# Performance work log

Hardware: AMD Instinct MI355X
Metric: run time of the kernel (lower is better)

The kernel has to match this reference:

```python
import jax, jax.numpy as jnp
import numpy as np

K, B, D, H = 8, 8192, 1024, 256


def setup_inputs() -> dict:
    key = jax.random.key(0)
    k_x, k_w1, k_w2 = jax.random.split(key, 3)
    x = jax.random.normal(k_x, (B, D), dtype=jnp.float32)
    # He-ish scaled weights so reconstructions stay finite
    W1 = jax.random.normal(k_w1, (K, D, H), dtype=jnp.float32) * (1.0 / np.sqrt(D))
    b1 = jnp.zeros((K, H), dtype=jnp.float32)
    W2 = jax.random.normal(k_w2, (K, H, D), dtype=jnp.float32) * (1.0 / np.sqrt(H))
    b2 = jnp.zeros((K, D), dtype=jnp.float32)
    return {"x": x, "W1": W1, "b1": b1, "W2": W2, "b2": b2}


def reference(x, W1, b1, W2, b2):
    # Run every expert AE on the full batch (matches predict()):
    h = jax.nn.relu(jnp.einsum('bd,kdh->kbh', x, W1) + b1[:, None, :])   # [K,B,H]
    recon = jnp.einsum('kbh,khd->kbd', h, W2) + b2[:, None, :]            # [K,B,D]
    # per-sample reconstruction MSE per expert
    err = jnp.mean((recon - x[None]) ** 2, axis=-1)                       # [K,B]
    # cluster_assignment = argmax over (-err) == argmin over err
    assign = jnp.argmin(err, axis=0)                                      # [B] int
    # gather-compute-scatter: select the winning expert's reconstruction
    x_out = recon[assign, jnp.arange(recon.shape[1])]                     # [B,D]
    return x_out
```

## Files before the change

kernel.cpp:

```cpp
#include <hip/hip_runtime.h>


#define KE 8
#define NB 8192
#define ND 1024
#define NH 256

typedef float f32x4 __attribute__((ext_vector_type(4)));
typedef short s16x8 __attribute__((ext_vector_type(8)));
typedef unsigned short u16x8 __attribute__((ext_vector_type(8)));
typedef unsigned short u16x4 __attribute__((ext_vector_type(4)));

__device__ __forceinline__ float bf2f(unsigned short h) {
  union { unsigned int u; float f; } v; v.u = ((unsigned int)h) << 16; return v.f;
}
__device__ __forceinline__ unsigned short f2bf(float f) {
  union { unsigned int u; float f; } v; v.f = f;
  unsigned int u = v.u;
  u += 0x7fffu + ((u >> 16) & 1u);
  return (unsigned short)(u >> 16);
}
__device__ __forceinline__ void split2(float x, unsigned short& hi, unsigned short& lo) {
  hi = f2bf(x);
  lo = f2bf(x - bf2f(hi));
}

__global__ __launch_bounds__(256) void pack_all(
    const float* __restrict__ W1, unsigned short* __restrict__ w1oh, unsigned short* __restrict__ w1ol,
    const float* __restrict__ W2, unsigned short* __restrict__ w2oh, unsigned short* __restrict__ w2ol,
    const float* __restrict__ xin, unsigned short* __restrict__ xoh, unsigned short* __restrict__ xol,
    unsigned int* __restrict__ cnt) {
  const int bx = blockIdx.x;
  const int tid = threadIdx.x;
  if (bx == 0 && tid < KE) cnt[tid] = 0;

  if (bx < 1024) {
    int gid = bx * 256 + tid;
    int L = gid & 63;
    int g = gid >> 6;
    int ks = g & 31;
    int ct = (g >> 5) & 15;
    int k = g >> 9;
    int col = ct * 16 + (L & 15);
    int kd0 = ks * 32 + (L >> 4) * 8;
    unsigned short th[8], tl[8];
#pragma unroll
    for (int j = 0; j < 8; ++j) {
      float v = W1[((size_t)k * ND + kd0 + j) * NH + col];
      split2(v, th[j], tl[j]);
    }
    size_t o = ((size_t)g * 64 + L) * 8;
    *(u16x8*)&w1oh[o] = *(u16x8*)th;
    *(u16x8*)&w1ol[o] = *(u16x8*)tl;
  } else if (bx < 2048) {
    int gid = (bx - 1024) * 256 + tid;
    int L = gid & 63;
    int g = gid >> 6;
    int ks = g & 7;
    int dt = (g >> 3) & 63;
    int k = g >> 9;
    int d2 = dt * 16 + (L & 15);
    int h0 = ks * 32 + (L >> 4) * 8;
    unsigned short th[8], tl[8];
#pragma unroll
    for (int j = 0; j < 8; ++j) {
      float v = W2[((size_t)k * NH + h0 + j) * ND + d2];
      split2(v, th[j], tl[j]);
    }
    size_t o = ((size_t)g * 64 + L) * 8;
    *(u16x8*)&w2oh[o] = *(u16x8*)th;
    *(u16x8*)&w2ol[o] = *(u16x8*)tl;
  } else {
    int gid = (bx - 2048) * 256 + tid;
    int L = gid & 63;
    int g = gid >> 6;
    int ks = g & 31;
    int rt = g >> 5;
    int row = rt * 16 + (L & 15);
    int kd0 = ks * 32 + (L >> 4) * 8;
    float4 a = *(const float4*)&xin[(size_t)row * ND + kd0];
    float4 b = *(const float4*)&xin[(size_t)row * ND + kd0 + 4];
    unsigned short th[8], tl[8];
    split2(a.x, th[0], tl[0]); split2(a.y, th[1], tl[1]);
    split2(a.z, th[2], tl[2]); split2(a.w, th[3], tl[3]);
    split2(b.x, th[4], tl[4]); split2(b.y, th[5], tl[5]);
    split2(b.z, th[6], tl[6]); split2(b.w, th[7], tl[7]);
    size_t o = ((size_t)g * 64 + L) * 8;
    *(u16x8*)&xoh[o] = *(u16x8*)th;
    *(u16x8*)&xol[o] = *(u16x8*)tl;
  }
}

#define LOAD_STAGE(ah, al, bh, bl, it)                  \
  do {                                                  \
    _Pragma("unroll")                                   \
    for (int q_ = 0; q_ < 4; ++q_) {                    \
      int o_ = xo[q_] + (it) * 512;                     \
      ah[q_] = *(const s16x8*)&xph[o_];                 \
      al[q_] = *(const s16x8*)&xpl[o_];                 \
    }                                                   \
    _Pragma("unroll")                                   \
    for (int q_ = 0; q_ < 4; ++q_) {                    \
      int o_ = wo1[q_] + (it) * 512;                    \
      bh[q_] = *(const s16x8*)&w1ph[o_];                \
      bl[q_] = *(const s16x8*)&w1pl[o_];                \
    }                                                   \
  } while (0)

#define MFMA_STAGE(ah, al, bh, bl)                                                                   \
  do {                                                                                               \
    _Pragma("unroll")                                                                                \
    for (int nt_ = 0; nt_ < 4; ++nt_)                                                                \
      _Pragma("unroll")                                                                              \
      for (int mt_ = 0; mt_ < 4; ++mt_) {                                                            \
        acc1[mt_][nt_] = __builtin_amdgcn_mfma_f32_16x16x32_bf16(ah[mt_], bh[nt_], acc1[mt_][nt_], 0, 0, 0); \
        acc1[mt_][nt_] = __builtin_amdgcn_mfma_f32_16x16x32_bf16(ah[mt_], bl[nt_], acc1[mt_][nt_], 0, 0, 0); \
        acc1[mt_][nt_] = __builtin_amdgcn_mfma_f32_16x16x32_bf16(al[mt_], bh[nt_], acc1[mt_][nt_], 0, 0, 0); \
      }                                                                                              \
  } while (0)

__global__ __launch_bounds__(256, 2) void ae_pass1(
    const unsigned short* __restrict__ xph, const unsigned short* __restrict__ xpl,
    const float* __restrict__ x,
    const unsigned short* __restrict__ w1ph, const unsigned short* __restrict__ w1pl,
    const float* __restrict__ b1,
    const unsigned short* __restrict__ w2ph, const unsigned short* __restrict__ w2pl,
    const float* __restrict__ b2, float* __restrict__ err) {
  __shared__ union {
    struct { unsigned short h[64][256]; unsigned short l[64][256]; } hs;
    float errp[4][64];
  } s;

  const int tid = threadIdx.x;
  const int wv = tid >> 6;
  const int lane = tid & 63;
  const int lo = lane & 15;
  const int quad = lane >> 4;
  const int k = blockIdx.x & 7;
  const int rtile = blockIdx.x >> 3;
  const int r0 = rtile * 64;

  int xo[4], wo1[4];
#pragma unroll
  for (int mt = 0; mt < 4; ++mt) xo[mt] = ((rtile * 4 + mt) * 32) * 512 + lane * 8;
#pragma unroll
  for (int nt = 0; nt < 4; ++nt) wo1[nt] = ((k * 16 + wv * 4 + nt) * 32) * 512 + lane * 8;

  f32x4 acc1[4][4];
#pragma unroll
  for (int mt = 0; mt < 4; ++mt)
#pragma unroll
    for (int nt = 0; nt < 4; ++nt) acc1[mt][nt] = (f32x4){0.f, 0.f, 0.f, 0.f};

  s16x8 Aah[4], Aal[4], Abh[4], Abl[4];
  s16x8 Bah[4], Bal[4], Bbh[4], Bbl[4];
  LOAD_STAGE(Aah, Aal, Abh, Abl, 0);
  LOAD_STAGE(Bah, Bal, Bbh, Bbl, 1);
  for (int it = 0; it < 32; it += 2) {
    MFMA_STAGE(Aah, Aal, Abh, Abl);
    if (it + 2 < 32) LOAD_STAGE(Aah, Aal, Abh, Abl, it + 2);
    MFMA_STAGE(Bah, Bal, Bbh, Bbl);
    if (it + 3 < 32) LOAD_STAGE(Bah, Bal, Bbh, Bbl, it + 3);
  }

#pragma unroll
  for (int nt = 0; nt < 4; ++nt) {
    float b1v = b1[(size_t)k * NH + wv * 64 + nt * 16 + lo];
#pragma unroll
    for (int mt = 0; mt < 4; ++mt)
#pragma unroll
      for (int i = 0; i < 4; ++i) {
        float v = acc1[mt][nt][i] + b1v;
        v = v > 0.f ? v : 0.f;
        unsigned short vh, vl;
        split2(v, vh, vl);
        int row = mt * 16 + quad * 4 + i, col = wv * 64 + nt * 16 + lo;
        int sc = col ^ ((row & 7) << 3);
        s.hs.h[row][sc] = vh;
        s.hs.l[row][sc] = vl;
      }
  }
  __syncthreads();

  float eacc[4][4];
#pragma unroll
  for (int mt = 0; mt < 4; ++mt)
#pragma unroll
    for (int i = 0; i < 4; ++i) eacc[mt][i] = 0.f;

  const int w2base = ((k * 64 + wv * 16) * 8) * 512 + lane * 8;

  for (int mc = 0; mc < 2; ++mc) {
    s16x8 hh[2][8], hl[2][8];
#pragma unroll
    for (int m2 = 0; m2 < 2; ++m2) {
      int row = (mc * 2 + m2) * 16 + lo;
      int rbase = row * 256;
      int sw = (row & 7) << 3;
#pragma unroll
      for (int ks = 0; ks < 8; ++ks) {
        int off = rbase + ((ks * 32 + quad * 8) ^ sw);
        hh[m2][ks] = *(const s16x8*)(&s.hs.h[0][0] + off);
        hl[m2][ks] = *(const s16x8*)(&s.hs.l[0][0] + off);
      }
    }
    for (int dt = 0; dt < 16; ++dt) {
      f32x4 acc2[2];
      acc2[0] = (f32x4){0.f, 0.f, 0.f, 0.f};
      acc2[1] = (f32x4){0.f, 0.f, 0.f, 0.f};
#pragma unroll
      for (int ks = 0; ks < 8; ++ks) {
        int wo = w2base + dt * 4096 + ks * 512;
        s16x8 bh = *(const s16x8*)&w2ph[wo];
        s16x8 bl = *(const s16x8*)&w2pl[wo];
#pragma unroll
        for (int m2 = 0; m2 < 2; ++m2) {
          acc2[m2] = __builtin_amdgcn_mfma_f32_16x16x32_bf16(hh[m2][ks], bh, acc2[m2], 0, 0, 0);
          acc2[m2] = __builtin_amdgcn_mfma_f32_16x16x32_bf16(hh[m2][ks], bl, acc2[m2], 0, 0, 0);
          acc2[m2] = __builtin_amdgcn_mfma_f32_16x16x32_bf16(hl[m2][ks], bh, acc2[m2], 0, 0, 0);
        }
      }
      const int d2 = wv * 256 + dt * 16 + lo;
      float b2v = b2[(size_t)k * ND + d2];
#pragma unroll
      for (int m2 = 0; m2 < 2; ++m2)
#pragma unroll
        for (int i = 0; i < 4; ++i) {
          int row = (mc * 2 + m2) * 16 + quad * 4 + i;
          float rec = acc2[m2][i] + b2v;
          float xv = x[(size_t)(r0 + row) * ND + d2];
          float dd = rec - xv;
          eacc[mc * 2 + m2][i] += dd * dd;
        }
    }
  }

  __syncthreads();
#pragma unroll
  for (int mt = 0; mt < 4; ++mt)
#pragma unroll
    for (int i = 0; i < 4; ++i) {
      float v = eacc[mt][i];
      v += __shfl_xor(v, 1, 16);
      v += __shfl_xor(v, 2, 16);
      v += __shfl_xor(v, 4, 16);
      v += __shfl_xor(v, 8, 16);
      if (lo == 0) s.errp[wv][mt * 16 + quad * 4 + i] = v;
    }
  __syncthreads();
  if (tid < 64)
    err[(size_t)k * NB + r0 + tid] =
        (s.errp[0][tid] + s.errp[1][tid] + s.errp[2][tid] + s.errp[3][tid]) * (1.0f / (float)ND);
}

__global__ __launch_bounds__(256) void ae_argmin(const float* __restrict__ err,
                                                 unsigned int* __restrict__ cnt,
                                                 int* __restrict__ bucket) {
  __shared__ unsigned int lc[KE];
  __shared__ unsigned int base[KE];
  int tid = threadIdx.x;
  if (tid < KE) lc[tid] = 0;
  __syncthreads();
  int b = blockIdx.x * 256 + tid;
  float best = err[b];
  int kmin = 0;
#pragma unroll
  for (int j = 1; j < KE; ++j) {
    float e = err[(size_t)j * NB + b];
    if (e < best) { best = e; kmin = j; }
  }
  unsigned int lpos = atomicAdd(&lc[kmin], 1u);
  __syncthreads();
  if (tid < KE) base[tid] = atomicAdd(&cnt[tid], lc[tid]);
  __syncthreads();
  bucket[(size_t)kmin * NB + (int)(base[kmin] + lpos)] = b;
}

__global__ __launch_bounds__(256) void ae_pass2(
    const float* __restrict__ x,
    const unsigned short* __restrict__ w1ph, const float* __restrict__ b1,
    const unsigned short* __restrict__ w2ph, const float* __restrict__ b2,
    const unsigned int* __restrict__ cnt, const int* __restrict__ bucket,
    float* __restrict__ out) {
  __shared__ unsigned short hs[64][NH + 8];
  __shared__ unsigned short xs[64][40];
  __shared__ int rid[64];

  const int k = blockIdx.x & 7;
  const int cv = (int)cnt[k];
  const int t0 = (blockIdx.x >> 3) * 64;
  if (t0 >= cv) return;
  const int nrows = min(64, cv - t0);

  const int tid = threadIdx.x;
  const int wv = tid >> 6;
  const int lane = tid & 63;
  const int lo = lane & 15;
  const int quad = lane >> 4;
  const int srow = tid >> 2, scol = (tid & 3) * 8;

  if (tid < 64) {
    int idx = t0 + tid;
    rid[tid] = bucket[(size_t)k * NB + (idx < cv ? idx : t0)];
  }
  __syncthreads();
  const int grow = rid[srow];

  f32x4 acc1[4][4];
#pragma unroll
  for (int mt = 0; mt < 4; ++mt)
#pragma unroll
    for (int nt = 0; nt < 4; ++nt) acc1[mt][nt] = (f32x4){0.f, 0.f, 0.f, 0.f};

  for (int it = 0; it < 32; ++it) {
    float4 xa = *(const float4*)&x[(size_t)grow * ND + it * 32 + scol];
    float4 xb = *(const float4*)&x[(size_t)grow * ND + it * 32 + scol + 4];
    s16x8 bfr[4];
#pragma unroll
    for (int nt = 0; nt < 4; ++nt)
      bfr[nt] = *(const s16x8*)&w1ph[(((size_t)(k * 16 + wv * 4 + nt) * 32) + it) * 512 + lane * 8];
    __syncthreads();
    unsigned short t[8];
    t[0] = f2bf(xa.x); t[1] = f2bf(xa.y); t[2] = f2bf(xa.z); t[3] = f2bf(xa.w);
    t[4] = f2bf(xb.x); t[5] = f2bf(xb.y); t[6] = f2bf(xb.z); t[7] = f2bf(xb.w);
    *(u16x8*)&xs[srow][scol] = *(u16x8*)t;
    __syncthreads();
    s16x8 af[4];
#pragma unroll
    for (int mt = 0; mt < 4; ++mt) af[mt] = *(const s16x8*)&xs[mt * 16 + lo][quad * 8];
#pragma unroll
    for (int mt = 0; mt < 4; ++mt)
#pragma unroll
      for (int nt = 0; nt < 4; ++nt)
        acc1[mt][nt] = __builtin_amdgcn_mfma_f32_16x16x32_bf16(af[mt], bfr[nt], acc1[mt][nt], 0, 0, 0);
  }
  __syncthreads();

#pragma unroll
  for (int nt = 0; nt < 4; ++nt) {
    float b1v = b1[(size_t)k * NH + wv * 64 + nt * 16 + lo];
#pragma unroll
    for (int mt = 0; mt < 4; ++mt)
#pragma unroll
      for (int i = 0; i < 4; ++i) {
        float v = acc1[mt][nt][i] + b1v;
        v = v > 0.f ? v : 0.f;
        hs[mt * 16 + quad * 4 + i][wv * 64 + nt * 16 + lo] = f2bf(v);
      }
  }
  __syncthreads();

  for (int c = 0; c < 32; ++c) {
    f32x4 acc2[2];
    acc2[0] = (f32x4){0.f, 0.f, 0.f, 0.f};
    acc2[1] = (f32x4){0.f, 0.f, 0.f, 0.f};
#pragma unroll
    for (int ks = 0; ks < 8; ++ks) {
      s16x8 af = *(const s16x8*)&hs[wv * 16 + lo][ks * 32 + quad * 8];
#pragma unroll
      for (int nt = 0; nt < 2; ++nt) {
        s16x8 bfr = *(const s16x8*)&w2ph[(((size_t)(k * 64 + c * 2 + nt) * 8) + ks) * 512 + lane * 8];
        acc2[nt] = __builtin_amdgcn_mfma_f32_16x16x32_bf16(af, bfr, acc2[nt], 0, 0, 0);
      }
    }
#pragma unroll
    for (int nt = 0; nt < 2; ++nt) {
      float b2v = b2[(size_t)k * ND + c * 32 + nt * 16 + lo];
#pragma unroll
      for (int i = 0; i < 4; ++i) {
        int row = wv * 16 + quad * 4 + i;
        if (row < nrows)
          out[(size_t)rid[row] * ND + c * 32 + nt * 16 + lo] = acc2[nt][i] + b2v;
      }
    }
  }
}

extern "C" void kernel_launch(void* const* d_in, const int* in_sizes, int n_in,
                              void* d_out, int out_size, void* d_ws, size_t ws_size,
                              hipStream_t stream) {
  (void)in_sizes; (void)n_in; (void)out_size; (void)ws_size;
  const float* x  = (const float*)d_in[0];
  const float* W1 = (const float*)d_in[1];
  const float* b1 = (const float*)d_in[2];
  const float* W2 = (const float*)d_in[3];
  const float* b2 = (const float*)d_in[4];
  float* out = (float*)d_out;

  char* ws = (char*)d_ws;
  const size_t szW = (size_t)KE * ND * NH * sizeof(unsigned short);
  const size_t szX = (size_t)NB * ND * sizeof(unsigned short);
  unsigned short* w1ph = (unsigned short*)(ws);
  unsigned short* w1pl = (unsigned short*)(ws + szW);
  unsigned short* w2ph = (unsigned short*)(ws + 2 * szW);
  unsigned short* w2pl = (unsigned short*)(ws + 3 * szW);
  unsigned short* xph  = (unsigned short*)(ws + 4 * szW);
  unsigned short* xpl  = (unsigned short*)(ws + 4 * szW + szX);
  char* tail           = ws + 4 * szW + 2 * szX;
  float* err           = (float*)tail;
  int* bucket          = (int*)(tail + (size_t)KE * NB * sizeof(float));
  unsigned int* cnt    = (unsigned int*)(tail + (size_t)KE * NB * sizeof(float)
                                         + (size_t)KE * NB * sizeof(int));

  pack_all<<<6144, 256, 0, stream>>>(W1, w1ph, w1pl, W2, w2ph, w2pl, x, xph, xpl, cnt);
  ae_pass1<<<1024, 256, 0, stream>>>(xph, xpl, x, w1ph, w1pl, b1, w2ph, w2pl, b2, err);
  ae_argmin<<<NB / 256, 256, 0, stream>>>(err, cnt, bucket);
  ae_pass2<<<1024, 256, 0, stream>>>(x, w1ph, b1, w2ph, b2, cnt, bucket, out);
}
```

Baseline: 427.8 us.

## Share x tiles via LDS staging in pass1 and widen pass2 x chunks

In pass1, each wave now loads only its own quarter of the packed x tile from global memory and writes it to an 8-slot LDS staging ring. All four waves then read the full tile from LDS, where before every wave loaded all four x row-tiles itself. The second GEMM now processes all 64 rows per W2 fetch, halving W2 global reads at the cost of more registers and per-iteration LDS reads. Pass2 converts x in 128-column chunks with fewer barriers and a larger LDS buffer.

```diff
diff --git a/kernel.cpp b/kernel.cpp
--- a/kernel.cpp
+++ b/kernel.cpp
@@ -9,7 +9,6 @@
 typedef float f32x4 __attribute__((ext_vector_type(4)));
 typedef short s16x8 __attribute__((ext_vector_type(8)));
 typedef unsigned short u16x8 __attribute__((ext_vector_type(8)));
-typedef unsigned short u16x4 __attribute__((ext_vector_type(4)));
 
 __device__ __forceinline__ float bf2f(unsigned short h) {
   union { unsigned int u; float f; } v; v.u = ((unsigned int)h) << 16; return v.f;
@@ -91,32 +90,59 @@
   }
 }
 
-#define LOAD_STAGE(ah, al, bh, bl, it)                  \
+#define LOADW1(bh, bl, it)                              \
+  do {                                                  \
+    _Pragma("unroll")                                   \
+    for (int nt_ = 0; nt_ < 4; ++nt_) {                 \
+      int o_ = wo1[nt_] + (it) * 512;                   \
+      bh[nt_] = *(const s16x8*)&w1ph[o_];               \
+      bl[nt_] = *(const s16x8*)&w1pl[o_];               \
+    }                                                   \
+  } while (0)
+
+#define GLOADX(itb)                                     \
   do {                                                  \
     _Pragma("unroll")                                   \
     for (int q_ = 0; q_ < 4; ++q_) {                    \
-      int o_ = xo[q_] + (it) * 512;                     \
-      ah[q_] = *(const s16x8*)&xph[o_];                 \
-      al[q_] = *(const s16x8*)&xpl[o_];                 \
-    }                                                   \
-    _Pragma("unroll")                                   \
-    for (int q_ = 0; q_ < 4; ++q_) {                    \
-      int o_ = wo1[q_] + (it) * 512;                    \
-      bh[q_] = *(const s16x8*)&w1ph[o_];                \
-      bl[q_] = *(const s16x8*)&w1pl[o_];                \
+      size_t go_ = xgbase + (size_t)((itb) + q_) * 512; \
+      xg[q_][0] = *(const s16x8*)&xph[go_];             \
+      xg[q_][1] = *(const s16x8*)&xpl[go_];             \
     }                                                   \
   } while (0)
 
-#define MFMA_STAGE(ah, al, bh, bl)                                                                   \
-  do {                                                                                               \
-    _Pragma("unroll")                                                                                \
-    for (int nt_ = 0; nt_ < 4; ++nt_)                                                                \
-      _Pragma("unroll")                                                                              \
-      for (int mt_ = 0; mt_ < 4; ++mt_) {                                                            \
-        acc1[mt_][nt_] = __builtin_amdgcn_mfma_f32_16x16x32_bf16(ah[mt_], bh[nt_], acc1[mt_][nt_], 0, 0, 0); \
-        acc1[mt_][nt_] = __builtin_amdgcn_mfma_f32_16x16x32_bf16(ah[mt_], bl[nt_], acc1[mt_][nt_], 0, 0, 0); \
-        acc1[mt_][nt_] = __builtin_amdgcn_mfma_f32_16x16x32_bf16(al[mt_], bh[nt_], acc1[mt_][nt_], 0, 0, 0); \
-      }                                                                                              \
+#define DSWRITEX(itb)                                        \
+  do {                                                       \
+    _Pragma("unroll")                                        \
+    for (int q_ = 0; q_ < 4; ++q_) {                         \
+      int sl_ = ((itb) + q_) & 7;                            \
+      *(s16x8*)&s.xstage[sl_][0][wv][lane * 8] = xg[q_][0];  \
+      *(s16x8*)&s.xstage[sl_][1][wv][lane * 8] = xg[q_][1];  \
+    }                                                        \
+  } while (0)
+
+#define MFMA_IT(xh, xl, Wh, Wl)                                                                        \
+  do {                                                                                                 \
+    _Pragma("unroll")                                                                                  \
+    for (int nt_ = 0; nt_ < 4; ++nt_)                                                                  \
+      _Pragma("unroll")                                                                                \
+      for (int mt_ = 0; mt_ < 4; ++mt_) {                                                              \
+        acc1[mt_][nt_] = __builtin_amdgcn_mfma_f32_16x16x32_bf16(xh[mt_], Wh[nt_], acc1[mt_][nt_], 0, 0, 0); \
+        acc1[mt_][nt_] = __builtin_amdgcn_mfma_f32_16x16x32_bf16(xh[mt_], Wl[nt_], acc1[mt_][nt_], 0, 0, 0); \
+        acc1[mt_][nt_] = __builtin_amdgcn_mfma_f32_16x16x32_bf16(xl[mt_], Wh[nt_], acc1[mt_][nt_], 0, 0, 0); \
+      }                                                                                                \
+  } while (0)
+
+#define SUBIT(itv, Wh, Wl)                                        \
+  do {                                                            \
+    s16x8 xh_[4], xl_[4];                                         \
+    int sl_ = (itv) & 7;                                          \
+    _Pragma("unroll")                                             \
+    for (int mt_ = 0; mt_ < 4; ++mt_) {                           \
+      xh_[mt_] = *(const s16x8*)&s.xstage[sl_][0][mt_][lane * 8]; \
+      xl_[mt_] = *(const s16x8*)&s.xstage[sl_][1][mt_][lane * 8]; \
+    }                                                             \
+    MFMA_IT(xh_, xl_, Wh, Wl);                                    \
+    if ((itv) + 2 < 32) LOADW1(Wh, Wl, (itv) + 2);                \
   } while (0)
 
 __global__ __launch_bounds__(256, 2) void ae_pass1(
@@ -128,6 +154,7 @@
     const float* __restrict__ b2, float* __restrict__ err) {
   __shared__ union {
     struct { unsigned short h[64][256]; unsigned short l[64][256]; } hs;
+    unsigned short xstage[8][2][4][512];
     float errp[4][64];
   } s;
 
@@ -140,11 +167,10 @@
   const int rtile = blockIdx.x >> 3;
   const int r0 = rtile * 64;
 
-  int xo[4], wo1[4];
-#pragma unroll
-  for (int mt = 0; mt < 4; ++mt) xo[mt] = ((rtile * 4 + mt) * 32) * 512 + lane * 8;
+  int wo1[4];
 #pragma unroll
   for (int nt = 0; nt < 4; ++nt) wo1[nt] = ((k * 16 + wv * 4 + nt) * 32) * 512 + lane * 8;
+  const size_t xgbase = ((size_t)(rtile * 4 + wv) * 32) * 512 + lane * 8;
 
   f32x4 acc1[4][4];
 #pragma unroll
@@ -152,15 +178,23 @@
 #pragma unroll
     for (int nt = 0; nt < 4; ++nt) acc1[mt][nt] = (f32x4){0.f, 0.f, 0.f, 0.f};
 
-  s16x8 Aah[4], Aal[4], Abh[4], Abl[4];
-  s16x8 Bah[4], Bal[4], Bbh[4], Bbl[4];
-  LOAD_STAGE(Aah, Aal, Abh, Abl, 0);
-  LOAD_STAGE(Bah, Bal, Bbh, Bbl, 1);
-  for (int it = 0; it < 32; it += 2) {
-    MFMA_STAGE(Aah, Aal, Abh, Abl);
-    if (it + 2 < 32) LOAD_STAGE(Aah, Aal, Abh, Abl, it + 2);
-    MFMA_STAGE(Bah, Bal, Bbh, Bbl);
-    if (it + 3 < 32) LOAD_STAGE(Bah, Bal, Bbh, Bbl, it + 3);
+  s16x8 xg[4][2];
+  s16x8 Ah[4], Al[4], Bh[4], Bl[4];
+  GLOADX(0);
+  LOADW1(Ah, Al, 0);
+  LOADW1(Bh, Bl, 1);
+  DSWRITEX(0);
+  __syncthreads();
+
+  for (int g = 0; g < 8; ++g) {
+    const int itb = g * 4;
+    if (g < 7) GLOADX(itb + 4);
+    SUBIT(itb + 0, Ah, Al);
+    SUBIT(itb + 1, Bh, Bl);
+    SUBIT(itb + 2, Ah, Al);
+    SUBIT(itb + 3, Bh, Bl);
+    if (g < 7) DSWRITEX(itb + 4);
+    __syncthreads();
   }
 
 #pragma unroll
@@ -182,6 +216,20 @@
   }
   __syncthreads();
 
+  s16x8 hh[2][8], hl[2][8];
+#pragma unroll
+  for (int m = 0; m < 2; ++m) {
+    int row = m * 16 + lo;
+    int rbase = row * 256;
+    int sw = (row & 7) << 3;
+#pragma unroll
+    for (int ks = 0; ks < 8; ++ks) {
+      int off = rbase + ((ks * 32 + quad * 8) ^ sw);
+      hh[m][ks] = *(const s16x8*)(&s.hs.h[0][0] + off);
+      hl[m][ks] = *(const s16x8*)(&s.hs.l[0][0] + off);
+    }
+  }
+
   float eacc[4][4];
 #pragma unroll
   for (int mt = 0; mt < 4; ++mt)
@@ -190,49 +238,46 @@
 
   const int w2base = ((k * 64 + wv * 16) * 8) * 512 + lane * 8;
 
-  for (int mc = 0; mc < 2; ++mc) {
-    s16x8 hh[2][8], hl[2][8];
-#pragma unroll
-    for (int m2 = 0; m2 < 2; ++m2) {
-      int row = (mc * 2 + m2) * 16 + lo;
-      int rbase = row * 256;
-      int sw = (row & 7) << 3;
-#pragma unroll
-      for (int ks = 0; ks < 8; ++ks) {
-        int off = rbase + ((ks * 32 + quad * 8) ^ sw);
-        hh[m2][ks] = *(const s16x8*)(&s.hs.h[0][0] + off);
-        hl[m2][ks] = *(const s16x8*)(&s.hs.l[0][0] + off);
-      }
-    }
-    for (int dt = 0; dt < 16; ++dt) {
-      f32x4 acc2[2];
-      acc2[0] = (f32x4){0.f, 0.f, 0.f, 0.f};
-      acc2[1] = (f32x4){0.f, 0.f, 0.f, 0.f};
-#pragma unroll
-      for (int ks = 0; ks < 8; ++ks) {
-        int wo = w2base + dt * 4096 + ks * 512;
-        s16x8 bh = *(const s16x8*)&w2ph[wo];
-        s16x8 bl = *(const s16x8*)&w2pl[wo];
-#pragma unroll
-        for (int m2 = 0; m2 < 2; ++m2) {
-          acc2[m2] = __builtin_amdgcn_mfma_f32_16x16x32_bf16(hh[m2][ks], bh, acc2[m2], 0, 0, 0);
-          acc2[m2] = __builtin_amdgcn_mfma_f32_16x16x32_bf16(hh[m2][ks], bl, acc2[m2], 0, 0, 0);
-          acc2[m2] = __builtin_amdgcn_mfma_f32_16x16x32_bf16(hl[m2][ks], bh, acc2[m2], 0, 0, 0);
-        }
-      }
-      const int d2 = wv * 256 + dt * 16 + lo;
-      float b2v = b2[(size_t)k * ND + d2];
-#pragma unroll
-      for (int m2 = 0; m2 < 2; ++m2)
-#pragma unroll
-        for (int i = 0; i < 4; ++i) {
-          int row = (mc * 2 + m2) * 16 + quad * 4 + i;
-          float rec = acc2[m2][i] + b2v;
-          float xv = x[(size_t)(r0 + row) * ND + d2];
-          float dd = rec - xv;
-          eacc[mc * 2 + m2][i] += dd * dd;
-        }
-    }
+  for (int dt = 0; dt < 16; ++dt) {
+    f32x4 acc2[4];
+#pragma unroll
+    for (int mt = 0; mt < 4; ++mt) acc2[mt] = (f32x4){0.f, 0.f, 0.f, 0.f};
+
+#pragma unroll
+    for (int ks = 0; ks < 8; ++ks) {
+      int wo = w2base + dt * 4096 + ks * 512;
+      s16x8 bh = *(const s16x8*)&w2ph[wo];
+      s16x8 bl = *(const s16x8*)&w2pl[wo];
+      s16x8 h2h[2], h2l[2];
+#pragma unroll
+      for (int m = 0; m < 2; ++m) {
+        int row = (2 + m) * 16 + lo;
+        int off = row * 256 + ((ks * 32 + quad * 8) ^ ((row & 7) << 3));
+        h2h[m] = *(const s16x8*)(&s.hs.h[0][0] + off);
+        h2l[m] = *(const s16x8*)(&s.hs.l[0][0] + off);
+      }
+#pragma unroll
+      for (int m = 0; m < 2; ++m) {
+        acc2[m] = __builtin_amdgcn_mfma_f32_16x16x32_bf16(hh[m][ks], bh, acc2[m], 0, 0, 0);
+        acc2[m] = __builtin_amdgcn_mfma_f32_16x16x32_bf16(hh[m][ks], bl, acc2[m], 0, 0, 0);
+        acc2[m] = __builtin_amdgcn_mfma_f32_16x16x32_bf16(hl[m][ks], bh, acc2[m], 0, 0, 0);
+        acc2[2 + m] = __builtin_amdgcn_mfma_f32_16x16x32_bf16(h2h[m], bh, acc2[2 + m], 0, 0, 0);
+        acc2[2 + m] = __builtin_amdgcn_mfma_f32_16x16x32_bf16(h2h[m], bl, acc2[2 + m], 0, 0, 0);
+        acc2[2 + m] = __builtin_amdgcn_mfma_f32_16x16x32_bf16(h2l[m], bh, acc2[2 + m], 0, 0, 0);
+      }
+    }
+    const int d2 = wv * 256 + dt * 16 + lo;
+    float b2v = b2[(size_t)k * ND + d2];
+#pragma unroll
+    for (int mt = 0; mt < 4; ++mt)
+#pragma unroll
+      for (int i = 0; i < 4; ++i) {
+        int row = mt * 16 + quad * 4 + i;
+        float rec = acc2[mt][i] + b2v;
+        float xv = x[(size_t)(r0 + row) * ND + d2];
+        float dd = rec - xv;
+        eacc[mt][i] += dd * dd;
+      }
   }
 
   __syncthreads();
@@ -283,7 +328,7 @@
     const unsigned int* __restrict__ cnt, const int* __restrict__ bucket,
     float* __restrict__ out) {
   __shared__ unsigned short hs[64][NH + 8];
-  __shared__ unsigned short xs[64][40];
+  __shared__ unsigned short xs[64][136];
   __shared__ int rid[64];
 
   const int k = blockIdx.x & 7;
@@ -312,27 +357,38 @@
 #pragma unroll
     for (int nt = 0; nt < 4; ++nt) acc1[mt][nt] = (f32x4){0.f, 0.f, 0.f, 0.f};
 
-  for (int it = 0; it < 32; ++it) {
-    float4 xa = *(const float4*)&x[(size_t)grow * ND + it * 32 + scol];
-    float4 xb = *(const float4*)&x[(size_t)grow * ND + it * 32 + scol + 4];
-    s16x8 bfr[4];
-#pragma unroll
-    for (int nt = 0; nt < 4; ++nt)
-      bfr[nt] = *(const s16x8*)&w1ph[(((size_t)(k * 16 + wv * 4 + nt) * 32) + it) * 512 + lane * 8];
+  for (int c = 0; c < 8; ++c) {
+    float4 xa[4], xb[4];
+#pragma unroll
+    for (int j = 0; j < 4; ++j) {
+      xa[j] = *(const float4*)&x[(size_t)grow * ND + c * 128 + j * 32 + scol];
+      xb[j] = *(const float4*)&x[(size_t)grow * ND + c * 128 + j * 32 + scol + 4];
+    }
     __syncthreads();
-    unsigned short t[8];
-    t[0] = f2bf(xa.x); t[1] = f2bf(xa.y); t[2] = f2bf(xa.z); t[3] = f2bf(xa.w);
-    t[4] = f2bf(xb.x); t[5] = f2bf(xb.y); t[6] = f2bf(xb.z); t[7] = f2bf(xb.w);
-    *(u16x8*)&xs[srow][scol] = *(u16x8*)t;
+#pragma unroll
+    for (int j = 0; j < 4; ++j) {
+      unsigned short t[8];
+      t[0] = f2bf(xa[j].x); t[1] = f2bf(xa[j].y); t[2] = f2bf(xa[j].z); t[3] = f2bf(xa[j].w);
+      t[4] = f2bf(xb[j].x); t[5] = f2bf(xb[j].y); t[6] = f2bf(xb[j].z); t[7] = f2bf(xb[j].w);
+      *(u16x8*)&xs[srow][j * 32 + scol] = *(u16x8*)t;
+    }
     __syncthreads();
-    s16x8 af[4];
-#pragma unroll
-    for (int mt = 0; mt < 4; ++mt) af[mt] = *(const s16x8*)&xs[mt * 16 + lo][quad * 8];
-#pragma unroll
-    for (int mt = 0; mt < 4; ++mt)
+#pragma unroll
+    for (int j = 0; j < 4; ++j) {
+      const int it = c * 4 + j;
+      s16x8 bfr[4];
 #pragma unroll
       for (int nt = 0; nt < 4; ++nt)
-        acc1[mt][nt] = __builtin_amdgcn_mfma_f32_16x16x32_bf16(af[mt], bfr[nt], acc1[mt][nt], 0, 0, 0);
+        bfr[nt] = *(const s16x8*)&w1ph[(((size_t)(k * 16 + wv * 4 + nt) * 32) + it) * 512 + lane * 8];
+      s16x8 af[4];
+#pragma unroll
+      for (int mt = 0; mt < 4; ++mt) af[mt] = *(const s16x8*)&xs[mt * 16 + lo][j * 32 + quad * 8];
+#pragma unroll
+      for (int mt = 0; mt < 4; ++mt)
+#pragma unroll
+        for (int nt = 0; nt < 4; ++nt)
+          acc1[mt][nt] = __builtin_amdgcn_mfma_f32_16x16x32_bf16(af[mt], bfr[nt], acc1[mt][nt], 0, 0, 0);
+    }
   }
   __syncthreads();
 
```

Result: slower. 633.3 us (+48.1%).

## Coalesce weight packing via LDS transpose and fuse pass1 second GEMM over all rows

Applied to the files above, without the earlier changes.

Weight packing for W1/W2 now loads coalesced float4 rows into a shared-memory tile and transposes from there, replacing strided scalar global reads. In pass1, the second GEMM now handles all 64 rows in one dt loop, so each W2 fragment is loaded from global memory once instead of twice. Rows 0-31 are held in registers and rows 32-63 are read from an LDS region pre-laid-out in MFMA fragment order. This cuts W2 global traffic but raises register pressure and adds LDS reads inside the inner loop.

```diff
diff --git a/kernel.cpp b/kernel.cpp
--- a/kernel.cpp
+++ b/kernel.cpp
@@ -9,7 +9,6 @@
 typedef float f32x4 __attribute__((ext_vector_type(4)));
 typedef short s16x8 __attribute__((ext_vector_type(8)));
 typedef unsigned short u16x8 __attribute__((ext_vector_type(8)));
-typedef unsigned short u16x4 __attribute__((ext_vector_type(4)));
 
 __device__ __forceinline__ float bf2f(unsigned short h) {
   union { unsigned int u; float f; } v; v.u = ((unsigned int)h) << 16; return v.f;
@@ -30,48 +29,51 @@
     const float* __restrict__ W2, unsigned short* __restrict__ w2oh, unsigned short* __restrict__ w2ol,
     const float* __restrict__ xin, unsigned short* __restrict__ xoh, unsigned short* __restrict__ xol,
     unsigned int* __restrict__ cnt) {
+  __shared__ float t[32][260];
   const int bx = blockIdx.x;
   const int tid = threadIdx.x;
   if (bx == 0 && tid < KE) cnt[tid] = 0;
 
-  if (bx < 1024) {
-    int gid = bx * 256 + tid;
-    int L = gid & 63;
-    int g = gid >> 6;
-    int ks = g & 31;
-    int ct = (g >> 5) & 15;
-    int k = g >> 9;
-    int col = ct * 16 + (L & 15);
-    int kd0 = ks * 32 + (L >> 4) * 8;
-    unsigned short th[8], tl[8];
-#pragma unroll
-    for (int j = 0; j < 8; ++j) {
-      float v = W1[((size_t)k * ND + kd0 + j) * NH + col];
-      split2(v, th[j], tl[j]);
-    }
-    size_t o = ((size_t)g * 64 + L) * 8;
-    *(u16x8*)&w1oh[o] = *(u16x8*)th;
-    *(u16x8*)&w1ol[o] = *(u16x8*)tl;
-  } else if (bx < 2048) {
-    int gid = (bx - 1024) * 256 + tid;
-    int L = gid & 63;
-    int g = gid >> 6;
-    int ks = g & 7;
-    int dt = (g >> 3) & 63;
-    int k = g >> 9;
-    int d2 = dt * 16 + (L & 15);
-    int h0 = ks * 32 + (L >> 4) * 8;
-    unsigned short th[8], tl[8];
-#pragma unroll
-    for (int j = 0; j < 8; ++j) {
-      float v = W2[((size_t)k * NH + h0 + j) * ND + d2];
-      split2(v, th[j], tl[j]);
-    }
-    size_t o = ((size_t)g * 64 + L) * 8;
-    *(u16x8*)&w2oh[o] = *(u16x8*)th;
-    *(u16x8*)&w2ol[o] = *(u16x8*)tl;
+  if (bx < 512) {
+    const bool isW1 = bx < 256;
+    const int b = isW1 ? bx : bx - 256;
+    int k, ks, q, CLEN, rowbase, c0;
+    const float* src;
+    unsigned short *oh, *ol;
+    if (isW1) {
+      k = b >> 5; ks = b & 31; q = 0;
+      CLEN = 256; rowbase = k * ND + ks * 32; c0 = 0;
+      src = W1; oh = w1oh; ol = w1ol;
+    } else {
+      k = b >> 5; ks = (b >> 2) & 7; q = b & 3;
+      CLEN = 1024; rowbase = k * NH + ks * 32; c0 = q * 256;
+      src = W2; oh = w2oh; ol = w2ol;
+    }
+#pragma unroll
+    for (int tl = 0; tl < 8; ++tl) {
+      int idx = tl * 256 + tid;
+      int r = idx >> 6;
+      int c4 = (idx & 63) * 4;
+      float4 v = *(const float4*)&src[(size_t)(rowbase + r) * CLEN + c0 + c4];
+      *(float4*)&t[r][c4] = v;
+    }
+    __syncthreads();
+#pragma unroll
+    for (int tl = 0; tl < 4; ++tl) {
+      int slot = tl * 256 + tid;
+      int ct = slot >> 6, l = slot & 63;
+      unsigned short th[8], tlw[8];
+#pragma unroll
+      for (int j = 0; j < 8; ++j)
+        split2(t[(l >> 4) * 8 + j][ct * 16 + (l & 15)], th[j], tlw[j]);
+      size_t g = isW1 ? ((size_t)(k * 16 + ct) * 32 + ks)
+                      : ((size_t)(k * 64 + q * 16 + ct) * 8 + ks);
+      size_t o = (g * 64 + l) * 8;
+      *(u16x8*)&oh[o] = *(u16x8*)th;
+      *(u16x8*)&ol[o] = *(u16x8*)tlw;
+    }
   } else {
-    int gid = (bx - 2048) * 256 + tid;
+    int gid = (bx - 512) * 256 + tid;
     int L = gid & 63;
     int g = gid >> 6;
     int ks = g & 31;
@@ -79,15 +81,15 @@
     int row = rt * 16 + (L & 15);
     int kd0 = ks * 32 + (L >> 4) * 8;
     float4 a = *(const float4*)&xin[(size_t)row * ND + kd0];
-    float4 b = *(const float4*)&xin[(size_t)row * ND + kd0 + 4];
-    unsigned short th[8], tl[8];
-    split2(a.x, th[0], tl[0]); split2(a.y, th[1], tl[1]);
-    split2(a.z, th[2], tl[2]); split2(a.w, th[3], tl[3]);
-    split2(b.x, th[4], tl[4]); split2(b.y, th[5], tl[5]);
-    split2(b.z, th[6], tl[6]); split2(b.w, th[7], tl[7]);
+    float4 b4 = *(const float4*)&xin[(size_t)row * ND + kd0 + 4];
+    unsigned short th[8], tlw[8];
+    split2(a.x, th[0], tlw[0]); split2(a.y, th[1], tlw[1]);
+    split2(a.z, th[2], tlw[2]); split2(a.w, th[3], tlw[3]);
+    split2(b4.x, th[4], tlw[4]); split2(b4.y, th[5], tlw[5]);
+    split2(b4.z, th[6], tlw[6]); split2(b4.w, th[7], tlw[7]);
     size_t o = ((size_t)g * 64 + L) * 8;
     *(u16x8*)&xoh[o] = *(u16x8*)th;
-    *(u16x8*)&xol[o] = *(u16x8*)tl;
+    *(u16x8*)&xol[o] = *(u16x8*)tlw;
   }
 }
 
@@ -127,7 +129,11 @@
     const unsigned short* __restrict__ w2ph, const unsigned short* __restrict__ w2pl,
     const float* __restrict__ b2, float* __restrict__ err) {
   __shared__ union {
-    struct { unsigned short h[64][256]; unsigned short l[64][256]; } hs;
+    struct {
+      unsigned short h[32][256];
+      unsigned short l[32][256];
+      unsigned short bf[4][8][512];
+    } hs;
     float errp[4][64];
   } s;
 
@@ -166,6 +172,9 @@
 #pragma unroll
   for (int nt = 0; nt < 4; ++nt) {
     float b1v = b1[(size_t)k * NH + wv * 64 + nt * 16 + lo];
+    const int ksb = wv * 2 + (nt >> 1);
+    const int lbase = 16 * (2 * (nt & 1) + (lo >> 3));
+    const int jj = lo & 7;
 #pragma unroll
     for (int mt = 0; mt < 4; ++mt)
 #pragma unroll
@@ -174,13 +183,34 @@
         v = v > 0.f ? v : 0.f;
         unsigned short vh, vl;
         split2(v, vh, vl);
-        int row = mt * 16 + quad * 4 + i, col = wv * 64 + nt * 16 + lo;
-        int sc = col ^ ((row & 7) << 3);
-        s.hs.h[row][sc] = vh;
-        s.hs.l[row][sc] = vl;
-      }
-  }
-  __syncthreads();
+        if (mt < 2) {
+          int row = mt * 16 + quad * 4 + i, col = wv * 64 + nt * 16 + lo;
+          int sc = col ^ ((row & 7) << 3);
+          s.hs.h[row][sc] = vh;
+          s.hs.l[row][sc] = vl;
+        } else {
+          int lp = (quad * 4 + i) + lbase;
+          int off = lp * 8 + jj;
+          s.hs.bf[(mt - 2) * 2 + 0][ksb][off] = vh;
+          s.hs.bf[(mt - 2) * 2 + 1][ksb][off] = vl;
+        }
+      }
+  }
+  __syncthreads();
+
+  s16x8 hh[2][8], hl[2][8];
+#pragma unroll
+  for (int m = 0; m < 2; ++m) {
+    int row = m * 16 + lo;
+    int rbase = row * 256;
+    int sw = (row & 7) << 3;
+#pragma unroll
+    for (int ks = 0; ks < 8; ++ks) {
+      int off = rbase + ((ks * 32 + quad * 8) ^ sw);
+      hh[m][ks] = *(const s16x8*)(&s.hs.h[0][0] + off);
+      hl[m][ks] = *(const s16x8*)(&s.hs.l[0][0] + off);
+    }
+  }
 
   float eacc[4][4];
 #pragma unroll
@@ -190,49 +220,44 @@
 
   const int w2base = ((k * 64 + wv * 16) * 8) * 512 + lane * 8;
 
-  for (int mc = 0; mc < 2; ++mc) {
-    s16x8 hh[2][8], hl[2][8];
-#pragma unroll
-    for (int m2 = 0; m2 < 2; ++m2) {
-      int row = (mc * 2 + m2) * 16 + lo;
-      int rbase = row * 256;
-      int sw = (row & 7) << 3;
-#pragma unroll
-      for (int ks = 0; ks < 8; ++ks) {
-        int off = rbase + ((ks * 32 + quad * 8) ^ sw);
-        hh[m2][ks] = *(const s16x8*)(&s.hs.h[0][0] + off);
-        hl[m2][ks] = *(const s16x8*)(&s.hs.l[0][0] + off);
-      }
-    }
-    for (int dt = 0; dt < 16; ++dt) {
-      f32x4 acc2[2];
-      acc2[0] = (f32x4){0.f, 0.f, 0.f, 0.f};
-      acc2[1] = (f32x4){0.f, 0.f, 0.f, 0.f};
-#pragma unroll
-      for (int ks = 0; ks < 8; ++ks) {
-        int wo = w2base + dt * 4096 + ks * 512;
-        s16x8 bh = *(const s16x8*)&w2ph[wo];
-        s16x8 bl = *(const s16x8*)&w2pl[wo];
-#pragma unroll
-        for (int m2 = 0; m2 < 2; ++m2) {
-          acc2[m2] = __builtin_amdgcn_mfma_f32_16x16x32_bf16(hh[m2][ks], bh, acc2[m2], 0, 0, 0);
-          acc2[m2] = __builtin_amdgcn_mfma_f32_16x16x32_bf16(hh[m2][ks], bl, acc2[m2], 0, 0, 0);
-          acc2[m2] = __builtin_amdgcn_mfma_f32_16x16x32_bf16(hl[m2][ks], bh, acc2[m2], 0, 0, 0);
-        }
-      }
-      const int d2 = wv * 256 + dt * 16 + lo;
-      float b2v = b2[(size_t)k * ND + d2];
-#pragma unroll
-      for (int m2 = 0; m2 < 2; ++m2)
-#pragma unroll
-        for (int i = 0; i < 4; ++i) {
-          int row = (mc * 2 + m2) * 16 + quad * 4 + i;
-          float rec = acc2[m2][i] + b2v;
-          float xv = x[(size_t)(r0 + row) * ND + d2];
-          float dd = rec - xv;
-          eacc[mc * 2 + m2][i] += dd * dd;
-        }
-    }
+  for (int dt = 0; dt < 16; ++dt) {
+    f32x4 acc2[4];
+#pragma unroll
+    for (int mt = 0; mt < 4; ++mt) acc2[mt] = (f32x4){0.f, 0.f, 0.f, 0.f};
+
+#pragma unroll
+    for (int ks = 0; ks < 8; ++ks) {
+      int wo = w2base + dt * 4096 + ks * 512;
+      s16x8 bh = *(const s16x8*)&w2ph[wo];
+      s16x8 bl = *(const s16x8*)&w2pl[wo];
+      s16x8 h2h[2], h2l[2];
+#pragma unroll
+      for (int m = 0; m < 2; ++m) {
+        h2h[m] = *(const s16x8*)&s.hs.bf[m * 2 + 0][ks][lane * 8];
+        h2l[m] = *(const s16x8*)&s.hs.bf[m * 2 + 1][ks][lane * 8];
+      }
+#pragma unroll
+      for (int m = 0; m < 2; ++m) {
+        acc2[m] = __builtin_amdgcn_mfma_f32_16x16x32_bf16(hh[m][ks], bh, acc2[m], 0, 0, 0);
+        acc2[m] = __builtin_amdgcn_mfma_f32_16x16x32_bf16(hh[m][ks], bl, acc2[m], 0, 0, 0);
+        acc2[m] = __builtin_amdgcn_mfma_f32_16x16x32_bf16(hl[m][ks], bh, acc2[m], 0, 0, 0);
+        acc2[2 + m] = __builtin_amdgcn_mfma_f32_16x16x32_bf16(h2h[m], bh, acc2[2 + m], 0, 0, 0);
+        acc2[2 + m] = __builtin_amdgcn_mfma_f32_16x16x32_bf16(h2h[m], bl, acc2[2 + m], 0, 0, 0);
+        acc2[2 + m] = __builtin_amdgcn_mfma_f32_16x16x32_bf16(h2l[m], bh, acc2[2 + m], 0, 0, 0);
+      }
+    }
+    const int d2 = wv * 256 + dt * 16 + lo;
+    float b2v = b2[(size_t)k * ND + d2];
+#pragma unroll
+    for (int mt = 0; mt < 4; ++mt)
+#pragma unroll
+      for (int i = 0; i < 4; ++i) {
+        int row = mt * 16 + quad * 4 + i;
+        float rec = acc2[mt][i] + b2v;
+        float xv = x[(size_t)(r0 + row) * ND + d2];
+        float dd = rec - xv;
+        eacc[mt][i] += dd * dd;
+      }
   }
 
   __syncthreads();
@@ -402,7 +427,7 @@
   unsigned int* cnt    = (unsigned int*)(tail + (size_t)KE * NB * sizeof(float)
                                          + (size_t)KE * NB * sizeof(int));
 
-  pack_all<<<6144, 256, 0, stream>>>(W1, w1ph, w1pl, W2, w2ph, w2pl, x, xph, xpl, cnt);
+  pack_all<<<4608, 256, 0, stream>>>(W1, w1ph, w1pl, W2, w2ph, w2pl, x, xph, xpl, cnt);
   ae_pass1<<<1024, 256, 0, stream>>>(xph, xpl, x, w1ph, w1pl, b1, w2ph, w2pl, b2, err);
   ae_argmin<<<NB / 256, 256, 0, stream>>>(err, cnt, bucket);
   ae_pass2<<<1024, 256, 0, stream>>>(x, w1ph, b1, w2ph, b2, cnt, bucket, out);
```

After: 611.0 us. 1.43x slower.

## Halve hidden LDS buffer, split W1 prefetch, raise occupancy to three blocks

Applied to the files above, without the earlier changes.

Shrinks the shared hidden-activation buffer from 64 to 32 rows by writing and consuming the hidden tile in two halves, with extra barriers between them. The first-GEMM prefetch now loads W1 fragments in two half-width chunks instead of a full double-buffered stage, which cuts live registers. Launch bounds rise from 2 to 3 blocks per SIMD, aiming for more latency hiding through occupancy. The cost is extra synchronisation, possible register spills, and a tighter software pipeline in the first GEMM.

```diff
diff --git a/kernel.cpp b/kernel.cpp
--- a/kernel.cpp
+++ b/kernel.cpp
@@ -9,7 +9,6 @@
 typedef float f32x4 __attribute__((ext_vector_type(4)));
 typedef short s16x8 __attribute__((ext_vector_type(8)));
 typedef unsigned short u16x8 __attribute__((ext_vector_type(8)));
-typedef unsigned short u16x4 __attribute__((ext_vector_type(4)));
 
 __device__ __forceinline__ float bf2f(unsigned short h) {
   union { unsigned int u; float f; } v; v.u = ((unsigned int)h) << 16; return v.f;
@@ -91,35 +90,61 @@
   }
 }
 
-#define LOAD_STAGE(ah, al, bh, bl, it)                  \
-  do {                                                  \
-    _Pragma("unroll")                                   \
-    for (int q_ = 0; q_ < 4; ++q_) {                    \
-      int o_ = xo[q_] + (it) * 512;                     \
-      ah[q_] = *(const s16x8*)&xph[o_];                 \
-      al[q_] = *(const s16x8*)&xpl[o_];                 \
-    }                                                   \
-    _Pragma("unroll")                                   \
-    for (int q_ = 0; q_ < 4; ++q_) {                    \
-      int o_ = wo1[q_] + (it) * 512;                    \
-      bh[q_] = *(const s16x8*)&w1ph[o_];                \
-      bl[q_] = *(const s16x8*)&w1pl[o_];                \
-    }                                                   \
+#define XLOAD(xh_, xl_, it)                         \
+  do {                                              \
+    _Pragma("unroll")                               \
+    for (int m_ = 0; m_ < 4; ++m_) {                \
+      int o_ = xo[m_] + (it) * 512;                 \
+      xh_[m_] = *(const s16x8*)&xph[o_];            \
+      xl_[m_] = *(const s16x8*)&xpl[o_];            \
+    }                                               \
   } while (0)
 
-#define MFMA_STAGE(ah, al, bh, bl)                                                                   \
-  do {                                                                                               \
-    _Pragma("unroll")                                                                                \
-    for (int nt_ = 0; nt_ < 4; ++nt_)                                                                \
-      _Pragma("unroll")                                                                              \
-      for (int mt_ = 0; mt_ < 4; ++mt_) {                                                            \
-        acc1[mt_][nt_] = __builtin_amdgcn_mfma_f32_16x16x32_bf16(ah[mt_], bh[nt_], acc1[mt_][nt_], 0, 0, 0); \
-        acc1[mt_][nt_] = __builtin_amdgcn_mfma_f32_16x16x32_bf16(ah[mt_], bl[nt_], acc1[mt_][nt_], 0, 0, 0); \
-        acc1[mt_][nt_] = __builtin_amdgcn_mfma_f32_16x16x32_bf16(al[mt_], bh[nt_], acc1[mt_][nt_], 0, 0, 0); \
-      }                                                                                              \
+#define WLOAD(wh_, wl_, it, c)                      \
+  do {                                              \
+    _Pragma("unroll")                               \
+    for (int j_ = 0; j_ < 2; ++j_) {                \
+      int o_ = wo1[(c)*2 + j_] + (it) * 512;        \
+      wh_[j_] = *(const s16x8*)&w1ph[o_];           \
+      wl_[j_] = *(const s16x8*)&w1pl[o_];           \
+    }                                               \
   } while (0)
 
-__global__ __launch_bounds__(256, 2) void ae_pass1(
+#define MFMA24(xh_, xl_, wh_, wl_, c)                                                                      \
+  do {                                                                                                     \
+    _Pragma("unroll")                                                                                      \
+    for (int j_ = 0; j_ < 2; ++j_)                                                                         \
+      _Pragma("unroll")                                                                                    \
+      for (int m_ = 0; m_ < 4; ++m_) {                                                                     \
+        acc1[m_][(c)*2+j_] = __builtin_amdgcn_mfma_f32_16x16x32_bf16(xh_[m_], wh_[j_], acc1[m_][(c)*2+j_], 0, 0, 0); \
+        acc1[m_][(c)*2+j_] = __builtin_amdgcn_mfma_f32_16x16x32_bf16(xh_[m_], wl_[j_], acc1[m_][(c)*2+j_], 0, 0, 0); \
+        acc1[m_][(c)*2+j_] = __builtin_amdgcn_mfma_f32_16x16x32_bf16(xl_[m_], wh_[j_], acc1[m_][(c)*2+j_], 0, 0, 0); \
+      }                                                                                                    \
+  } while (0)
+
+#define EPIPART(mt0)                                                        \
+  do {                                                                      \
+    _Pragma("unroll")                                                       \
+    for (int nt_ = 0; nt_ < 4; ++nt_) {                                     \
+      float b1v_ = b1[(size_t)k * NH + wv * 64 + nt_ * 16 + lo];            \
+      _Pragma("unroll")                                                     \
+      for (int mm_ = 0; mm_ < 2; ++mm_)                                     \
+        _Pragma("unroll")                                                   \
+        for (int i_ = 0; i_ < 4; ++i_) {                                    \
+          float v_ = acc1[(mt0) + mm_][nt_][i_] + b1v_;                     \
+          v_ = v_ > 0.f ? v_ : 0.f;                                         \
+          unsigned short vh_, vl_;                                          \
+          split2(v_, vh_, vl_);                                             \
+          int rl_ = mm_ * 16 + quad * 4 + i_;                               \
+          int col_ = wv * 64 + nt_ * 16 + lo;                               \
+          int sc_ = col_ ^ ((rl_ & 7) << 3);                                \
+          s.hx.h[rl_][sc_] = vh_;                                           \
+          s.hx.l[rl_][sc_] = vl_;                                           \
+        }                                                                   \
+    }                                                                       \
+  } while (0)
+
+__global__ __launch_bounds__(256, 3) void ae_pass1(
     const unsigned short* __restrict__ xph, const unsigned short* __restrict__ xpl,
     const float* __restrict__ x,
     const unsigned short* __restrict__ w1ph, const unsigned short* __restrict__ w1pl,
@@ -127,7 +152,7 @@
     const unsigned short* __restrict__ w2ph, const unsigned short* __restrict__ w2pl,
     const float* __restrict__ b2, float* __restrict__ err) {
   __shared__ union {
-    struct { unsigned short h[64][256]; unsigned short l[64][256]; } hs;
+    struct { unsigned short h[32][256]; unsigned short l[32][256]; } hx;
     float errp[4][64];
   } s;
 
@@ -152,87 +177,122 @@
 #pragma unroll
     for (int nt = 0; nt < 4; ++nt) acc1[mt][nt] = (f32x4){0.f, 0.f, 0.f, 0.f};
 
-  s16x8 Aah[4], Aal[4], Abh[4], Abl[4];
-  s16x8 Bah[4], Bal[4], Bbh[4], Bbl[4];
-  LOAD_STAGE(Aah, Aal, Abh, Abl, 0);
-  LOAD_STAGE(Bah, Bal, Bbh, Bbl, 1);
+  s16x8 XAh[4], XAl[4], XBh[4], XBl[4];
+  s16x8 W0h[2], W0l[2], W1h_[2], W1l_[2];
+  XLOAD(XAh, XAl, 0);
+  WLOAD(W0h, W0l, 0, 0);
   for (int it = 0; it < 32; it += 2) {
-    MFMA_STAGE(Aah, Aal, Abh, Abl);
-    if (it + 2 < 32) LOAD_STAGE(Aah, Aal, Abh, Abl, it + 2);
-    MFMA_STAGE(Bah, Bal, Bbh, Bbl);
-    if (it + 3 < 32) LOAD_STAGE(Bah, Bal, Bbh, Bbl, it + 3);
-  }
-
-#pragma unroll
-  for (int nt = 0; nt < 4; ++nt) {
-    float b1v = b1[(size_t)k * NH + wv * 64 + nt * 16 + lo];
-#pragma unroll
-    for (int mt = 0; mt < 4; ++mt)
+    XLOAD(XBh, XBl, it + 1);
+    WLOAD(W1h_, W1l_, it, 1);
+    MFMA24(XAh, XAl, W0h, W0l, 0);
+    WLOAD(W0h, W0l, it + 1, 0);
+    MFMA24(XAh, XAl, W1h_, W1l_, 1);
+    if (it + 2 < 32) XLOAD(XAh, XAl, it + 2);
+    WLOAD(W1h_, W1l_, it + 1, 1);
+    MFMA24(XBh, XBl, W0h, W0l, 0);
+    if (it + 2 < 32) WLOAD(W0h, W0l, it + 2, 0);
+    MFMA24(XBh, XBl, W1h_, W1l_, 1);
+  }
+
+  float eacc[4][4];
+#pragma unroll
+  for (int mt = 0; mt < 4; ++mt)
+#pragma unroll
+    for (int i = 0; i < 4; ++i) eacc[mt][i] = 0.f;
+
+  const int w2base = ((k * 64 + wv * 16) * 8) * 512 + lane * 8;
+
+  EPIPART(0);
+  __syncthreads();
+
+  s16x8 hh[2][8], hl[2][8];
+#pragma unroll
+  for (int m2 = 0; m2 < 2; ++m2) {
+    int row = m2 * 16 + lo;
+    int rbase = row * 256;
+    int sw = (row & 7) << 3;
+#pragma unroll
+    for (int ks = 0; ks < 8; ++ks) {
+      int off = rbase + ((ks * 32 + quad * 8) ^ sw);
+      hh[m2][ks] = *(const s16x8*)(&s.hx.h[0][0] + off);
+      hl[m2][ks] = *(const s16x8*)(&s.hx.l[0][0] + off);
+    }
+  }
+  __syncthreads();
+  EPIPART(2);
+  __syncthreads();
+
+  for (int dt = 0; dt < 16; ++dt) {
+    f32x4 acc2[2];
+    acc2[0] = (f32x4){0.f, 0.f, 0.f, 0.f};
+    acc2[1] = (f32x4){0.f, 0.f, 0.f, 0.f};
+#pragma unroll
+    for (int ks = 0; ks < 8; ++ks) {
+      int wo = w2base + dt * 4096 + ks * 512;
+      s16x8 bh = *(const s16x8*)&w2ph[wo];
+      s16x8 bl = *(const s16x8*)&w2pl[wo];
+#pragma unroll
+      for (int m2 = 0; m2 < 2; ++m2) {
+        acc2[m2] = __builtin_amdgcn_mfma_f32_16x16x32_bf16(hh[m2][ks], bh, acc2[m2], 0, 0, 0);
+        acc2[m2] = __builtin_amdgcn_mfma_f32_16x16x32_bf16(hh[m2][ks], bl, acc2[m2], 0, 0, 0);
+        acc2[m2] = __builtin_amdgcn_mfma_f32_16x16x32_bf16(hl[m2][ks], bh, acc2[m2], 0, 0, 0);
+      }
+    }
+    const int d2 = wv * 256 + dt * 16 + lo;
+    float b2v = b2[(size_t)k * ND + d2];
+#pragma unroll
+    for (int m2 = 0; m2 < 2; ++m2)
 #pragma unroll
       for (int i = 0; i < 4; ++i) {
-        float v = acc1[mt][nt][i] + b1v;
-        v = v > 0.f ? v : 0.f;
-        unsigned short vh, vl;
-        split2(v, vh, vl);
-        int row = mt * 16 + quad * 4 + i, col = wv * 64 + nt * 16 + lo;
-        int sc = col ^ ((row & 7) << 3);
-        s.hs.h[row][sc] = vh;
-        s.hs.l[row][sc] = vl;
-      }
-  }
-  __syncthreads();
-
-  float eacc[4][4];
-#pragma unroll
-  for (int mt = 0; mt < 4; ++mt)
-#pragma unroll
-    for (int i = 0; i < 4; ++i) eacc[mt][i] = 0.f;
-
-  const int w2base = ((k * 64 + wv * 16) * 8) * 512 + lane * 8;
-
-  for (int mc = 0; mc < 2; ++mc) {
-    s16x8 hh[2][8], hl[2][8];
-#pragma unroll
-    for (int m2 = 0; m2 < 2; ++m2) {
-      int row = (mc * 2 + m2) * 16 + lo;
-      int rbase = row * 256;
-      int sw = (row & 7) << 3;
-#pragma unroll
-      for (int ks = 0; ks < 8; ++ks) {
-        int off = rbase + ((ks * 32 + quad * 8) ^ sw);
-        hh[m2][ks] = *(const s16x8*)(&s.hs.h[0][0] + off);
-        hl[m2][ks] = *(const s16x8*)(&s.hs.l[0][0] + off);
-      }
-    }
-    for (int dt = 0; dt < 16; ++dt) {
-      f32x4 acc2[2];
-      acc2[0] = (f32x4){0.f, 0.f, 0.f, 0.f};
-      acc2[1] = (f32x4){0.f, 0.f, 0.f, 0.f};
-#pragma unroll
-      for (int ks = 0; ks < 8; ++ks) {
-        int wo = w2base + dt * 4096 + ks * 512;
-        s16x8 bh = *(const s16x8*)&w2ph[wo];
-        s16x8 bl = *(const s16x8*)&w2pl[wo];
-#pragma unroll
-        for (int m2 = 0; m2 < 2; ++m2) {
-          acc2[m2] = __builtin_amdgcn_mfma_f32_16x16x32_bf16(hh[m2][ks], bh, acc2[m2], 0, 0, 0);
-          acc2[m2] = __builtin_amdgcn_mfma_f32_16x16x32_bf16(hh[m2][ks], bl, acc2[m2], 0, 0, 0);
-          acc2[m2] = __builtin_amdgcn_mfma_f32_16x16x32_bf16(hl[m2][ks], bh, acc2[m2], 0, 0, 0);
-        }
-      }
-      const int d2 = wv * 256 + dt * 16 + lo;
-      float b2v = b2[(size_t)k * ND + d2];
-#pragma unroll
-      for (int m2 = 0; m2 < 2; ++m2)
-#pragma unroll
-        for (int i = 0; i < 4; ++i) {
-          int row = (mc * 2 + m2) * 16 + quad * 4 + i;
-          float rec = acc2[m2][i] + b2v;
-          float xv = x[(size_t)(r0 + row) * ND + d2];
-          float dd = rec - xv;
-          eacc[mc * 2 + m2][i] += dd * dd;
-        }
-    }
+        int row = m2 * 16 + quad * 4 + i;
+        float rec = acc2[m2][i] + b2v;
+        float xv = x[(size_t)(r0 + row) * ND + d2];
+        float dd = rec - xv;
+        eacc[m2][i] += dd * dd;
+      }
+  }
+
+#pragma unroll
+  for (int m2 = 0; m2 < 2; ++m2) {
+    int row = m2 * 16 + lo;
+    int rbase = row * 256;
+    int sw = (row & 7) << 3;
+#pragma unroll
+    for (int ks = 0; ks < 8; ++ks) {
+      int off = rbase + ((ks * 32 + quad * 8) ^ sw);
+      hh[m2][ks] = *(const s16x8*)(&s.hx.h[0][0] + off);
+      hl[m2][ks] = *(const s16x8*)(&s.hx.l[0][0] + off);
+    }
+  }
+
+  for (int dt = 0; dt < 16; ++dt) {
+    f32x4 acc2[2];
+    acc2[0] = (f32x4){0.f, 0.f, 0.f, 0.f};
+    acc2[1] = (f32x4){0.f, 0.f, 0.f, 0.f};
+#pragma unroll
+    for (int ks = 0; ks < 8; ++ks) {
+      int wo = w2base + dt * 4096 + ks * 512;
+      s16x8 bh = *(const s16x8*)&w2ph[wo];
+      s16x8 bl = *(const s16x8*)&w2pl[wo];
+#pragma unroll
+      for (int m2 = 0; m2 < 2; ++m2) {
+        acc2[m2] = __builtin_amdgcn_mfma_f32_16x16x32_bf16(hh[m2][ks], bh, acc2[m2], 0, 0, 0);
+        acc2[m2] = __builtin_amdgcn_mfma_f32_16x16x32_bf16(hh[m2][ks], bl, acc2[m2], 0, 0, 0);
+        acc2[m2] = __builtin_amdgcn_mfma_f32_16x16x32_bf16(hl[m2][ks], bh, acc2[m2], 0, 0, 0);
+      }
+    }
+    const int d2 = wv * 256 + dt * 16 + lo;
+    float b2v = b2[(size_t)k * ND + d2];
+#pragma unroll
+    for (int m2 = 0; m2 < 2; ++m2)
+#pragma unroll
+      for (int i = 0; i < 4; ++i) {
+        int row = 32 + m2 * 16 + quad * 4 + i;
+        float rec = acc2[m2][i] + b2v;
+        float xv = x[(size_t)(r0 + row) * ND + d2];
+        float dd = rec - xv;
+        eacc[2 + m2][i] += dd * dd;
+      }
   }
 
   __syncthreads();
```

New measurement: 723.9 us. 69.2% more time.
